# Optimization experiments

Measured on AMD Instinct MI355X. Metric: run time of the kernel, lower is better.

Reference implementation:

```python
import jax, jax.numpy as jnp
import numpy as np

EPS = 1e-5  # torch LayerNorm default


def setup_inputs() -> dict:
    key = jax.random.key(0)
    k_x, k_wc, k_w = jax.random.split(key, 3)
    B, S, D = 16, 512, 2048
    x = jax.random.normal(k_x, (B, S, D), dtype=jnp.float32)
    # LayerNorm params
    gamma = jnp.ones((D,), dtype=jnp.float32)
    beta = jnp.zeros((D,), dtype=jnp.float32)
    # router (spatial_cls) Linear(d_ffn, 4)
    Wc = jax.random.normal(k_wc, (D, 4), dtype=jnp.float32) * 0.02
    bc = jnp.zeros((4,), dtype=jnp.float32)
    # 4 pointwise Conv1d experts: kernel size 1 over seq channels -> [4, S, S]
    W = jax.random.normal(k_w, (4, S, S), dtype=jnp.float32) * (1.0 / np.sqrt(S))
    # biases initialised to constants -1.0, -0.5, 0.5, 1.0 per expert
    b = jnp.stack([
        jnp.full((S,), -1.0, dtype=jnp.float32),
        jnp.full((S,), -0.5, dtype=jnp.float32),
        jnp.full((S,), 0.5, dtype=jnp.float32),
        jnp.full((S,), 1.0, dtype=jnp.float32),
    ])
    return {"x": x, "gamma": gamma, "beta": beta, "Wc": Wc, "bc": bc, "W": W, "b": b}


def reference(x, gamma, beta, Wc, bc, W, b):
    # LayerNorm over last dim
    mu = jnp.mean(x, axis=-1, keepdims=True)
    var = jnp.mean(jnp.square(x - mu), axis=-1, keepdims=True)
    y = (x - mu) * jax.lax.rsqrt(var + EPS) * gamma + beta
    # router: computed as in the original, but (faithfully to the source bug)
    # NOT used for dispatch -- dispatch uses the batch index n, clamped to 3.
    cls = jax.nn.softmax(y[:, 0] @ Wc + bc, axis=-1)
    _cls_idx = jnp.argmax(cls, axis=-1)  # computed, unused (original bug)
    eidx = jnp.minimum(jnp.arange(x.shape[0]), 3)  # sample n -> expert min(n,3)
    # pointwise Conv1d == seq-mixing matmul: out[b,s,d] = sum_t W_e[s,t] y[b,t,d] + b_e[s]
    out = jnp.einsum('bst,btd->bsd', W[eidx], y) + b[eidx][:, :, None]
    return jax.nn.gelu(out, approximate=False) + x
```

## Files before the change

kernel.cpp:

```cpp
#include <hip/hip_runtime.h>
#include <hip/hip_bf16.h>
#include <math.h>

#define NB 16
#define NS 512
#define ND 2048

typedef __attribute__((ext_vector_type(4))) float  f32x4v;
typedef __attribute__((ext_vector_type(8))) short  short8v;
typedef __attribute__((ext_vector_type(4))) float  accv;

__device__ __forceinline__ unsigned short f2bf(float f) {
  union { float f; unsigned u; } v; v.f = f;
  unsigned r = v.u + 0x7FFFu + ((v.u >> 16) & 1u);
  return (unsigned short)(r >> 16);
}

__global__ __launch_bounds__(256) void k_meanvar(const float* __restrict__ x,
                                                 float* __restrict__ mv) {
  int row = blockIdx.x;
  const float* xr = x + (size_t)row * ND;
  int tid = threadIdx.x;
  float s = 0.f, ss = 0.f;
#pragma unroll
  for (int i = 0; i < 2; ++i) {
    f32x4v v = *reinterpret_cast<const f32x4v*>(xr + tid * 8 + i * 4);
#pragma unroll
    for (int j = 0; j < 4; ++j) { s += v[j]; ss += v[j] * v[j]; }
  }
#pragma unroll
  for (int off = 32; off > 0; off >>= 1) {
    s  += __shfl_down(s, off);
    ss += __shfl_down(ss, off);
  }
  __shared__ float red[8];
  int wid = tid >> 6, lane = tid & 63;
  if (lane == 0) { red[wid * 2] = s; red[wid * 2 + 1] = ss; }
  __syncthreads();
  if (tid == 0) {
    float S1 = red[0] + red[2] + red[4] + red[6];
    float S2 = red[1] + red[3] + red[5] + red[7];
    float mean = S1 * (1.0f / ND);
    float var  = S2 * (1.0f / ND) - mean * mean;
    mv[2 * row]     = mean;
    mv[2 * row + 1] = rsqrtf(var + 1e-5f);
  }
}

__global__ __launch_bounds__(256) void k_normT(const float* __restrict__ x,
                                               const float* __restrict__ mv,
                                               const float* __restrict__ gamma,
                                               const float* __restrict__ beta,
                                               unsigned short* __restrict__ yT) {
  int d0 = blockIdx.x * 64, t0 = blockIdx.y * 64, bb = blockIdx.z;
  __shared__ unsigned int lds[64 * 32];
  int tid = threadIdx.x;
  {
    int tl = tid >> 2;
    int c  = tid & 3;
    int trow = bb * NS + t0 + tl;
    float mean = mv[2 * trow], rstd = mv[2 * trow + 1];
    const float* xr = x + (size_t)trow * ND + d0;
    int k = tl & 31;
#pragma unroll
    for (int q = 0; q < 4; ++q) {
      int dl = c * 16 + q * 4;
      f32x4v v = *reinterpret_cast<const f32x4v*>(xr + dl);
      f32x4v g = *reinterpret_cast<const f32x4v*>(gamma + d0 + dl);
      f32x4v b = *reinterpret_cast<const f32x4v*>(beta + d0 + dl);
      unsigned short h[4];
#pragma unroll
      for (int j = 0; j < 4; ++j) h[j] = f2bf((v[j] - mean) * rstd * g[j] + b[j]);
      lds[tl * 32 + (((dl >> 1)    ) ^ k)] = (unsigned)h[0] | ((unsigned)h[1] << 16);
      lds[tl * 32 + (((dl >> 1) + 1) ^ k)] = (unsigned)h[2] | ((unsigned)h[3] << 16);
    }
  }
  __syncthreads();
  {
    int dl = tid >> 2;
    int tc = (tid & 3) * 16;
    short8v o0, o1;
#pragma unroll
    for (int i = 0; i < 16; ++i) {
      int t = tc + i;
      unsigned w = lds[t * 32 + ((dl >> 1) ^ (t & 31))];
      unsigned short val = (dl & 1) ? (unsigned short)(w >> 16)
                                    : (unsigned short)(w & 0xffffu);
      if (i < 8) o0[i] = (short)val; else o1[i - 8] = (short)val;
    }
    size_t base = ((size_t)bb * ND + d0 + dl) * NS + t0 + tc;
    *reinterpret_cast<short8v*>(yT + base)     = o0;
    *reinterpret_cast<short8v*>(yT + base + 8) = o1;
  }
}

#define APITCH 40
__global__ __launch_bounds__(256) void k_gemm(const unsigned short* __restrict__ yT,
                                              const float* __restrict__ W,
                                              const float* __restrict__ bias,
                                              const float* __restrict__ x,
                                              float* __restrict__ out) {
  int n0 = blockIdx.x * 128, m0 = blockIdx.y * 128, bb = blockIdx.z;
  int e = bb < 3 ? bb : 3;
  const float* Wp          = W  + (size_t)e  * NS * NS;
  const unsigned short* Bp = yT + (size_t)bb * ND * NS;
  __shared__ unsigned short Alds[128 * APITCH];
  __shared__ unsigned short Blds[128 * APITCH];
  int tid = threadIdx.x;
  int lane = tid & 63, wid = tid >> 6;
  int wr = wid >> 1, wc = wid & 1;
  accv acc[4][4] = {};

  int lr = lane & 15, lk = (lane >> 4) * 8;

  for (int k0 = 0; k0 < NS; k0 += 32) {
    {
      int colq  = (tid & 7) * 4;
      int rbase = tid >> 3;
#pragma unroll
      for (int p = 0; p < 4; ++p) {
        int r = rbase + p * 32;
        f32x4v v = *reinterpret_cast<const f32x4v*>(Wp + (size_t)(m0 + r) * NS + k0 + colq);
        unsigned lo = (unsigned)f2bf(v[0]) | ((unsigned)f2bf(v[1]) << 16);
        unsigned hi = (unsigned)f2bf(v[2]) | ((unsigned)f2bf(v[3]) << 16);
        uint2 pk; pk.x = lo; pk.y = hi;
        *reinterpret_cast<uint2*>(&Alds[r * APITCH + colq]) = pk;
      }
    }
    {
      int co    = (tid & 3) * 8;
      int rbase = tid >> 2;
#pragma unroll
      for (int p = 0; p < 2; ++p) {
        int r = rbase + p * 64;
        short8v v = *reinterpret_cast<const short8v*>(Bp + (size_t)(n0 + r) * NS + k0 + co);
        *reinterpret_cast<short8v*>(&Blds[r * APITCH + co]) = v;
      }
    }
    __syncthreads();

    short8v a[4], b[4];
#pragma unroll
    for (int mi = 0; mi < 4; ++mi)
      a[mi] = *reinterpret_cast<const short8v*>(&Alds[(wr * 64 + mi * 16 + lr) * APITCH + lk]);
#pragma unroll
    for (int ni = 0; ni < 4; ++ni)
      b[ni] = *reinterpret_cast<const short8v*>(&Blds[(wc * 64 + ni * 16 + lr) * APITCH + lk]);
#pragma unroll
    for (int mi = 0; mi < 4; ++mi)
#pragma unroll
      for (int ni = 0; ni < 4; ++ni)
        acc[mi][ni] = __builtin_amdgcn_mfma_f32_16x16x32_bf16(a[mi], b[ni], acc[mi][ni], 0, 0, 0);
    __syncthreads();
  }

  const float* bp = bias + (size_t)e * NS;
#pragma unroll
  for (int mi = 0; mi < 4; ++mi) {
#pragma unroll
    for (int ni = 0; ni < 4; ++ni) {
#pragma unroll
      for (int r = 0; r < 4; ++r) {
        int s = m0 + wr * 64 + mi * 16 + ((lane >> 4) * 4) + r;
        int d = n0 + wc * 64 + ni * 16 + (lane & 15);
        float v = acc[mi][ni][r] + bp[s];
        float g = 0.5f * v * (1.0f + erff(v * 0.70710678118f));
        size_t idx = ((size_t)bb * NS + s) * ND + d;
        out[idx] = g + x[idx];
      }
    }
  }
}

extern "C" void kernel_launch(void* const* d_in, const int* in_sizes, int n_in,
                              void* d_out, int out_size, void* d_ws, size_t ws_size,
                              hipStream_t stream) {
  const float* x     = (const float*)d_in[0];
  const float* gamma = (const float*)d_in[1];
  const float* beta  = (const float*)d_in[2];
  const float* W     = (const float*)d_in[5];
  const float* bias  = (const float*)d_in[6];
  float* out = (float*)d_out;

  unsigned short* yT = (unsigned short*)d_ws;
  float* mv = (float*)((char*)d_ws + (size_t)NB * ND * NS * 2);

  k_meanvar<<<NB * NS, 256, 0, stream>>>(x, mv);
  k_normT<<<dim3(ND / 64, NS / 64, NB), 256, 0, stream>>>(x, mv, gamma, beta, yT);
  k_gemm<<<dim3(ND / 128, NS / 128, NB), 256, 0, stream>>>(yT, W, bias, x, out);
}
```

Before: 212.6 us.

## Pre-tile swizzled bf16 operand images and load GEMM tiles via global_load_lds

W is now converted to bf16 once in a separate kernel, and the normalized activations are written into pre-tiled, XOR-swizzled 128x32 images. This lets the GEMM stream each k-slice straight into LDS with global_load_lds, with no per-iteration fp32 conversion and no register staging. The row-stats kernel now uses one wave per row with xor shuffles, which removes the LDS reduction and the block barrier. The exact erf GELU is replaced with the tanh approximation written in sigmoid form, which trades exactness against the reference for cheaper math.

```diff
diff --git a/kernel.cpp b/kernel.cpp
--- a/kernel.cpp
+++ b/kernel.cpp
@@ -16,34 +16,54 @@
   return (unsigned short)(r >> 16);
 }
 
+__device__ __forceinline__ int swz(int r, int kq) { return r * 4 + (kq ^ ((r >> 1) & 3)); }
+
+#define GLL16(gp, lp) __builtin_amdgcn_global_load_lds(                        \
+    (const __attribute__((address_space(1))) void*)(gp),                       \
+    (__attribute__((address_space(3))) void*)(lp), 16, 0, 0)
+
 __global__ __launch_bounds__(256) void k_meanvar(const float* __restrict__ x,
                                                  float* __restrict__ mv) {
-  int row = blockIdx.x;
+  int row  = blockIdx.x * 4 + (threadIdx.x >> 6);
+  int lane = threadIdx.x & 63;
   const float* xr = x + (size_t)row * ND;
-  int tid = threadIdx.x;
   float s = 0.f, ss = 0.f;
 #pragma unroll
-  for (int i = 0; i < 2; ++i) {
-    f32x4v v = *reinterpret_cast<const f32x4v*>(xr + tid * 8 + i * 4);
+  for (int q = 0; q < 8; ++q) {
+    f32x4v v = *reinterpret_cast<const f32x4v*>(xr + q * 256 + lane * 4);
 #pragma unroll
     for (int j = 0; j < 4; ++j) { s += v[j]; ss += v[j] * v[j]; }
   }
 #pragma unroll
-  for (int off = 32; off > 0; off >>= 1) {
-    s  += __shfl_down(s, off);
-    ss += __shfl_down(ss, off);
-  }
-  __shared__ float red[8];
-  int wid = tid >> 6, lane = tid & 63;
-  if (lane == 0) { red[wid * 2] = s; red[wid * 2 + 1] = ss; }
-  __syncthreads();
-  if (tid == 0) {
-    float S1 = red[0] + red[2] + red[4] + red[6];
-    float S2 = red[1] + red[3] + red[5] + red[7];
-    float mean = S1 * (1.0f / ND);
-    float var  = S2 * (1.0f / ND) - mean * mean;
+  for (int off = 1; off < 64; off <<= 1) {
+    s  += __shfl_xor(s, off);
+    ss += __shfl_xor(ss, off);
+  }
+  if (lane == 0) {
+    float mean = s * (1.0f / ND);
+    float var  = ss * (1.0f / ND) - mean * mean;
     mv[2 * row]     = mean;
     mv[2 * row + 1] = rsqrtf(var + 1e-5f);
+  }
+}
+
+__global__ __launch_bounds__(256) void k_wcvt(const float* __restrict__ W,
+                                              unsigned short* __restrict__ Aimg) {
+  int ks = blockIdx.x, mp = blockIdx.y, e = blockIdx.z;
+  size_t img = ((size_t)(e * 4 + mp) * 16 + ks) * 4096;
+  int tid = threadIdx.x;
+#pragma unroll
+  for (int u = 0; u < 2; ++u) {
+    int p = u * 256 + tid;
+    int r = p >> 2, cc = p & 3;
+    int kq = cc ^ ((r >> 1) & 3);
+    const float* src = W + ((size_t)e * NS + mp * 128 + r) * NS + ks * 32 + kq * 8;
+    f32x4v v0 = *reinterpret_cast<const f32x4v*>(src);
+    f32x4v v1 = *reinterpret_cast<const f32x4v*>(src + 4);
+    short8v o;
+#pragma unroll
+    for (int j = 0; j < 4; ++j) { o[j] = (short)f2bf(v0[j]); o[4 + j] = (short)f2bf(v1[j]); }
+    *reinterpret_cast<short8v*>(Aimg + img + (size_t)p * 8) = o;
   }
 }
 
@@ -51,7 +71,7 @@
                                                const float* __restrict__ mv,
                                                const float* __restrict__ gamma,
                                                const float* __restrict__ beta,
-                                               unsigned short* __restrict__ yT) {
+                                               unsigned short* __restrict__ Bimg) {
   int d0 = blockIdx.x * 64, t0 = blockIdx.y * 64, bb = blockIdx.z;
   __shared__ unsigned int lds[64 * 32];
   int tid = threadIdx.x;
@@ -88,64 +108,53 @@
                                     : (unsigned short)(w & 0xffffu);
       if (i < 8) o0[i] = (short)val; else o1[i - 8] = (short)val;
     }
-    size_t base = ((size_t)bb * ND + d0 + dl) * NS + t0 + tc;
-    *reinterpret_cast<short8v*>(yT + base)     = o0;
-    *reinterpret_cast<short8v*>(yT + base + 8) = o1;
-  }
-}
-
-#define APITCH 40
-__global__ __launch_bounds__(256) void k_gemm(const unsigned short* __restrict__ yT,
-                                              const float* __restrict__ W,
+    int d  = d0 + dl;
+    int np = d >> 7, r = d & 127;
+    int tb  = t0 + tc;
+    int ks  = tb >> 5;
+    int kq0 = (tb >> 3) & 3;
+    size_t img = ((size_t)(bb * 16 + np) * 16 + ks) * 4096;
+    *reinterpret_cast<short8v*>(Bimg + img + (size_t)swz(r, kq0)     * 8) = o0;
+    *reinterpret_cast<short8v*>(Bimg + img + (size_t)swz(r, kq0 + 1) * 8) = o1;
+  }
+}
+
+__global__ __launch_bounds__(256) void k_gemm(const unsigned short* __restrict__ Aimg,
+                                              const unsigned short* __restrict__ Bimg,
                                               const float* __restrict__ bias,
                                               const float* __restrict__ x,
                                               float* __restrict__ out) {
-  int n0 = blockIdx.x * 128, m0 = blockIdx.y * 128, bb = blockIdx.z;
+  int np = blockIdx.x, mp = blockIdx.y, bb = blockIdx.z;
   int e = bb < 3 ? bb : 3;
-  const float* Wp          = W  + (size_t)e  * NS * NS;
-  const unsigned short* Bp = yT + (size_t)bb * ND * NS;
-  __shared__ unsigned short Alds[128 * APITCH];
-  __shared__ unsigned short Blds[128 * APITCH];
+  const char* Abase = (const char*)(Aimg + ((size_t)(e  * 4 + mp) * 16) * 4096);
+  const char* Bbase = (const char*)(Bimg + ((size_t)(bb * 16 + np) * 16) * 4096);
+  __shared__ unsigned short Al[4096];
+  __shared__ unsigned short Bl[4096];
   int tid = threadIdx.x;
   int lane = tid & 63, wid = tid >> 6;
   int wr = wid >> 1, wc = wid & 1;
+  int lr = lane & 15, kq = lane >> 4;
+
+  int aoff[4], boff[4];
+#pragma unroll
+  for (int mi = 0; mi < 4; ++mi) { int rr = wr * 64 + mi * 16 + lr; aoff[mi] = swz(rr, kq) * 8; }
+#pragma unroll
+  for (int ni = 0; ni < 4; ++ni) { int rr = wc * 64 + ni * 16 + lr; boff[ni] = swz(rr, kq) * 8; }
+
   accv acc[4][4] = {};
 
-  int lr = lane & 15, lk = (lane >> 4) * 8;
-
-  for (int k0 = 0; k0 < NS; k0 += 32) {
-    {
-      int colq  = (tid & 7) * 4;
-      int rbase = tid >> 3;
-#pragma unroll
-      for (int p = 0; p < 4; ++p) {
-        int r = rbase + p * 32;
-        f32x4v v = *reinterpret_cast<const f32x4v*>(Wp + (size_t)(m0 + r) * NS + k0 + colq);
-        unsigned lo = (unsigned)f2bf(v[0]) | ((unsigned)f2bf(v[1]) << 16);
-        unsigned hi = (unsigned)f2bf(v[2]) | ((unsigned)f2bf(v[3]) << 16);
-        uint2 pk; pk.x = lo; pk.y = hi;
-        *reinterpret_cast<uint2*>(&Alds[r * APITCH + colq]) = pk;
-      }
-    }
-    {
-      int co    = (tid & 3) * 8;
-      int rbase = tid >> 2;
-#pragma unroll
-      for (int p = 0; p < 2; ++p) {
-        int r = rbase + p * 64;
-        short8v v = *reinterpret_cast<const short8v*>(Bp + (size_t)(n0 + r) * NS + k0 + co);
-        *reinterpret_cast<short8v*>(&Blds[r * APITCH + co]) = v;
-      }
+  for (int ks = 0; ks < 16; ++ks) {
+#pragma unroll
+    for (int i = 0; i < 2; ++i) {
+      GLL16(Abase + ks * 8192 + i * 4096 + tid * 16, (char*)Al + i * 4096 + wid * 1024);
+      GLL16(Bbase + ks * 8192 + i * 4096 + tid * 16, (char*)Bl + i * 4096 + wid * 1024);
     }
     __syncthreads();
-
     short8v a[4], b[4];
 #pragma unroll
-    for (int mi = 0; mi < 4; ++mi)
-      a[mi] = *reinterpret_cast<const short8v*>(&Alds[(wr * 64 + mi * 16 + lr) * APITCH + lk]);
-#pragma unroll
-    for (int ni = 0; ni < 4; ++ni)
-      b[ni] = *reinterpret_cast<const short8v*>(&Blds[(wc * 64 + ni * 16 + lr) * APITCH + lk]);
+    for (int mi = 0; mi < 4; ++mi) a[mi] = *reinterpret_cast<const short8v*>(&Al[aoff[mi]]);
+#pragma unroll
+    for (int ni = 0; ni < 4; ++ni) b[ni] = *reinterpret_cast<const short8v*>(&Bl[boff[ni]]);
 #pragma unroll
     for (int mi = 0; mi < 4; ++mi)
 #pragma unroll
@@ -155,6 +164,7 @@
   }
 
   const float* bp = bias + (size_t)e * NS;
+  int m0 = mp * 128, n0 = np * 128;
 #pragma unroll
   for (int mi = 0; mi < 4; ++mi) {
 #pragma unroll
@@ -164,7 +174,8 @@
         int s = m0 + wr * 64 + mi * 16 + ((lane >> 4) * 4) + r;
         int d = n0 + wc * 64 + ni * 16 + (lane & 15);
         float v = acc[mi][ni][r] + bp[s];
-        float g = 0.5f * v * (1.0f + erff(v * 0.70710678118f));
+        float u = 1.5957691216f * (v + 0.044715f * v * v * v);
+        float g = v / (1.0f + __expf(-u));
         size_t idx = ((size_t)bb * NS + s) * ND + d;
         out[idx] = g + x[idx];
       }
@@ -182,10 +193,12 @@
   const float* bias  = (const float*)d_in[6];
   float* out = (float*)d_out;
 
-  unsigned short* yT = (unsigned short*)d_ws;
-  float* mv = (float*)((char*)d_ws + (size_t)NB * ND * NS * 2);
-
-  k_meanvar<<<NB * NS, 256, 0, stream>>>(x, mv);
-  k_normT<<<dim3(ND / 64, NS / 64, NB), 256, 0, stream>>>(x, mv, gamma, beta, yT);
-  k_gemm<<<dim3(ND / 128, NS / 128, NB), 256, 0, stream>>>(yT, W, bias, x, out);
-}
+  unsigned short* Aimg = (unsigned short*)d_ws;
+  float*          mv   = (float*)((char*)d_ws + (2ull << 20));
+  unsigned short* Bimg = (unsigned short*)((char*)d_ws + (2ull << 20) + (64ull << 10));
+
+  k_meanvar<<<NB * NS / 4, 256, 0, stream>>>(x, mv);
+  k_wcvt<<<dim3(16, 4, 4), 256, 0, stream>>>(W, Aimg);
+  k_normT<<<dim3(ND / 64, NS / 64, NB), 256, 0, stream>>>(x, mv, gamma, beta, Bimg);
+  k_gemm<<<dim3(ND / 128, NS / 128, NB), 256, 0, stream>>>(Aimg, Bimg, bias, x, out);
+}
```

Measured after the change: 177.0 us. 1.2x faster.
